# Optimization experiments

Measured on AMD Instinct MI355X. Metric: run time of the kernel, lower is better.

The kernel has to match this reference:

```python
import jax, jax.numpy as jnp
import numpy as np
import math

B, N, E, H, MLP_H = 4, 1024, 768, 12, 1536
D = E // H
EPS = 1e-6


def clayernorm(x, gamma, beta):
    # x: [..., E, 2]
    real, imag = x[..., 0], x[..., 1]
    mag = jnp.sqrt(real * real + imag * imag + EPS)
    mean = jnp.mean(mag, axis=-1, keepdims=True)
    var = jnp.mean((mag - mean) ** 2, axis=-1, keepdims=True)
    scale = ((mag - mean) / jnp.sqrt(var + EPS)) / (mag + EPS)
    out_r = gamma[:, 0] * (real * scale) + beta[:, 0]
    out_i = gamma[:, 1] * (imag * scale) + beta[:, 1]
    return jnp.stack([out_r, out_i], axis=-1)


def clinear(x, wr, wi, br, bi):
    # x: [..., in, 2]; wr/wi: [out, in]
    xr, xi = x[..., 0], x[..., 1]
    out_r = xr @ wr.T - xi @ wi.T + br
    out_i = xr @ wi.T + xi @ wr.T + bi
    return jnp.stack([out_r, out_i], axis=-1)


def cgelu(x):
    return jnp.stack([jax.nn.gelu(x[..., 0], approximate=False),
                      jax.nn.gelu(x[..., 1], approximate=False)], axis=-1)


def setup_inputs() -> dict:
    key = jax.random.key(0)
    ks = jax.random.split(key, 8)
    std_qkv = math.sqrt(2.0 / (E + 3 * E))
    std_proj = math.sqrt(2.0 / (E + E))
    std_m1 = math.sqrt(2.0 / (E + MLP_H))
    std_m2 = math.sqrt(2.0 / (MLP_H + E))
    return {
        "x": jax.random.normal(ks[0], (B, N, 2 * E), dtype=jnp.float32),
        "g1": jnp.ones((E, 2), jnp.float32), "b1": jnp.zeros((E, 2), jnp.float32),
        "g2": jnp.ones((E, 2), jnp.float32), "b2": jnp.zeros((E, 2), jnp.float32),
        "qkv_wr": std_qkv * jax.random.normal(ks[1], (3 * E, E), jnp.float32),
        "qkv_wi": std_qkv * jax.random.normal(ks[2], (3 * E, E), jnp.float32),
        "qkv_br": jnp.zeros((3 * E,), jnp.float32), "qkv_bi": jnp.zeros((3 * E,), jnp.float32),
        "proj_wr": std_proj * jax.random.normal(ks[3], (E, E), jnp.float32),
        "proj_wi": std_proj * jax.random.normal(ks[4], (E, E), jnp.float32),
        "proj_br": jnp.zeros((E,), jnp.float32), "proj_bi": jnp.zeros((E,), jnp.float32),
        "m1_wr": std_m1 * jax.random.normal(ks[5], (MLP_H, E), jnp.float32),
        "m1_wi": std_m1 * jax.random.normal(ks[6], (MLP_H, E), jnp.float32),
        "m1_br": jnp.zeros((MLP_H,), jnp.float32), "m1_bi": jnp.zeros((MLP_H,), jnp.float32),
        "m2_wr": std_m2 * jax.random.normal(ks[7], (E, MLP_H), jnp.float32),
        "m2_wi": std_m2 * jax.random.normal(jax.random.fold_in(key, 9), (E, MLP_H), jnp.float32),
        "m2_br": jnp.zeros((E,), jnp.float32), "m2_bi": jnp.zeros((E,), jnp.float32),
    }


def _forward(x, g1, b1, g2, b2, qkv_wr, qkv_wi, qkv_br, qkv_bi,
             proj_wr, proj_wi, proj_br, proj_bi,
             m1_wr, m1_wi, m1_br, m1_bi, m2_wr, m2_wi, m2_br, m2_bi):
    xc = x.reshape(B, N, E, 2)
    xn = clayernorm(xc, g1, b1)
    qkv = clinear(xn, qkv_wr, qkv_wi, qkv_br, qkv_bi)      # [B,N,3E,2]
    qkv = qkv.reshape(B, N, 3, H, D, 2).transpose(2, 0, 3, 1, 4, 5)  # [3,B,H,N,D,2]
    q, k, v = qkv[0], qkv[1], qkv[2]
    qr, qi = q[..., 0], q[..., 1]
    kr, ki = k[..., 0], k[..., 1]
    attn_r = jnp.einsum('bhqd,bhkd->bhqk', qr, kr) + jnp.einsum('bhqd,bhkd->bhqk', qi, ki)
    attn_i = jnp.einsum('bhqd,bhkd->bhqk', qr, ki) - jnp.einsum('bhqd,bhkd->bhqk', qi, kr)
    mag = jnp.sqrt(attn_r * attn_r + attn_i * attn_i + 1e-8) / math.sqrt(D)
    w = jax.nn.softmax(mag, axis=-1)
    out_r = jnp.einsum('bhqk,bhkd->bhqd', w, v[..., 0])
    out_i = jnp.einsum('bhqk,bhkd->bhqd', w, v[..., 1])
    attn_out = jnp.stack([out_r, out_i], axis=-1)           # [B,H,N,D,2]
    attn_out = attn_out.transpose(0, 2, 1, 3, 4).reshape(B, N, E, 2)
    attn_out = clinear(attn_out, proj_wr, proj_wi, proj_br, proj_bi)
    xc = xc + attn_out
    xn2 = clayernorm(xc, g2, b2)
    h = clinear(xn2, m1_wr, m1_wi, m1_br, m1_bi)
    h = cgelu(h)
    mlp_out = clinear(h, m2_wr, m2_wi, m2_br, m2_bi)
    xc = xc + mlp_out
    return xc.reshape(B, N, 2 * E)


def reference(x, g1, b1, g2, b2, qkv_wr, qkv_wi, qkv_br, qkv_bi,
              proj_wr, proj_wi, proj_br, proj_bi,
              m1_wr, m1_wi, m1_br, m1_bi, m2_wr, m2_wi, m2_br, m2_bi):
    return _forward(x, g1, b1, g2, b2, qkv_wr, qkv_wi, qkv_br, qkv_bi,
                    proj_wr, proj_wi, proj_br, proj_bi,
                    m1_wr, m1_wi, m1_br, m1_bi, m2_wr, m2_wi, m2_br, m2_bi)
```

## Files before the change

kernel.cpp:

```cpp
#include <hip/hip_runtime.h>
#include <math.h>

#define BB 4
#define NN 1024
#define EE 768
#define HH 12
#define DD 64
#define MLPH 1536
#define RR (BB*NN)
#define SZH ((size_t)48*1024*64)

constexpr float EPS = 1e-6f;

typedef __bf16 bf16_t;
typedef bf16_t bf16x8 __attribute__((ext_vector_type(8)));
typedef bf16_t bf16x4 __attribute__((ext_vector_type(4)));
typedef float  f32x4  __attribute__((ext_vector_type(4)));
typedef unsigned short us8 __attribute__((ext_vector_type(8)));

#define MFMA16 __builtin_amdgcn_mfma_f32_16x16x32_bf16

__device__ __forceinline__ float gelu_exact(float x){
  return 0.5f * x * (1.0f + erff(x * 0.70710678118654752440f));
}

__device__ __forceinline__ bf16x8 negv(bf16x8 v){
  us8 u = __builtin_bit_cast(us8, v);
  u ^= (unsigned short)0x8000;
  return __builtin_bit_cast(bf16x8, u);
}

__device__ __forceinline__ void split2(float f, bf16_t& h, bf16_t& l){
  h = (bf16_t)f; l = (bf16_t)(f - (float)h);
}

__device__ __forceinline__ void cvtstore(bf16_t* hp, bf16_t* lp, f32x4 v){
  bf16x4 h, l;
  #pragma unroll
  for (int i=0;i<4;i++){
    float f = v[i];
    bf16_t hb = (bf16_t)f;
    h[i] = hb;
    l[i] = (bf16_t)(f - (float)hb);
  }
  *(bf16x4*)hp = h;
  *(bf16x4*)lp = l;
}

__device__ __forceinline__ void gload_lds16(const bf16_t* g, bf16_t* l){
  __builtin_amdgcn_global_load_lds(
      (const __attribute__((address_space(1))) void*)g,
      (__attribute__((address_space(3))) void*)l, 16, 0, 0);
}

__device__ __forceinline__ size_t tiled_ad(int r, int c, int Ko){
  return (((size_t)(r>>4)*Ko + (c>>3))*16 + (r&15))*8 + (c&7);
}

__global__ __launch_bounds__(256) void cln_kernel(
    const float* __restrict__ inI,
    const float* __restrict__ inR, const float* __restrict__ inIm,
    const float* __restrict__ gamma, const float* __restrict__ beta,
    bf16_t* __restrict__ out4, int mode)
{
  const size_t PS = (size_t)RR*EE;
  int row = blockIdx.x;
  int t = threadIdx.x;
  __shared__ float sbuf[4];
  float vr[3], vi[3], mg[3];
  #pragma unroll
  for (int j=0;j<3;j++){
    int e = t + 256*j;
    float a, b;
    if (mode == 0){
      a = inI[(size_t)row*(2*EE) + 2*e];
      b = inI[(size_t)row*(2*EE) + 2*e + 1];
    } else {
      a = inR[(size_t)row*EE + e];
      b = inIm[(size_t)row*EE + e];
    }
    vr[j]=a; vi[j]=b;
    mg[j] = sqrtf(a*a + b*b + EPS);
  }
  int lane = t & 63, wv = t >> 6;
  float s = mg[0]+mg[1]+mg[2];
  #pragma unroll
  for (int o=32;o>0;o>>=1) s += __shfl_down(s, o, 64);
  if (lane==0) sbuf[wv] = s;
  __syncthreads();
  float mean = (sbuf[0]+sbuf[1]+sbuf[2]+sbuf[3]) * (1.0f/EE);
  __syncthreads();
  float v = 0.f;
  #pragma unroll
  for (int j=0;j<3;j++){ float d = mg[j]-mean; v += d*d; }
  #pragma unroll
  for (int o=32;o>0;o>>=1) v += __shfl_down(v, o, 64);
  if (lane==0) sbuf[wv] = v;
  __syncthreads();
  float var = (sbuf[0]+sbuf[1]+sbuf[2]+sbuf[3]) * (1.0f/EE);
  float inv = 1.0f / sqrtf(var + EPS);
  #pragma unroll
  for (int j=0;j<3;j++){
    int e = t + 256*j;
    float scale = ((mg[j]-mean) * inv) / (mg[j] + EPS);
    float oR = gamma[2*e]   * (vr[j]*scale) + beta[2*e];
    float oI = gamma[2*e+1] * (vi[j]*scale) + beta[2*e+1];
    bf16_t hR,lR,hI,lI;
    split2(oR,hR,lR); split2(oI,hI,lI);
    size_t ad = tiled_ad(row, e, 96);
    out4[ad]        = hR;
    out4[PS + ad]   = lR;
    out4[2*PS + ad] = hI;
    out4[3*PS + ad] = lI;
  }
}

template<int ACT, int RES_MODE, int OUT_MODE>
__global__ __launch_bounds__(256, 3) void cgemm_v3(
    const bf16_t* __restrict__ a4,
    const float* __restrict__ wr, const float* __restrict__ wi,
    const float* __restrict__ br_, const float* __restrict__ bi_,
    const float* __restrict__ resr, const float* __restrict__ resi,
    float* __restrict__ outr, float* __restrict__ outi,
    bf16_t* __restrict__ osplit,
    int K, int OUT)
{
  __shared__ bf16_t Al[16384];
  __shared__ bf16_t Bl[8192];

  const int tid = threadIdx.x;
  const int wid = tid >> 6, lane = tid & 63;
  const int rowBase = blockIdx.y * 128, colBase = blockIdx.x * 64;
  const int Ko = K >> 3;
  const size_t AS = (size_t)RR * K;

  const int b_so = (tid >> 4) & 3;
  const int b_se = (tid & 1) * 4;
  const int b_r0 = ((tid & 15) >> 1) + 8*wid;

  const int fr = lane & 15, fq = lane >> 4;
  const int wr0 = (wid >> 1) * 64, wc0 = (wid & 1) * 32;

  f32x4 accR[4][2], accI[4][2];
  #pragma unroll
  for (int mi=0;mi<4;mi++)
    #pragma unroll
    for (int ni=0;ni<2;ni++){ accR[mi][ni] = (f32x4)0.f; accI[mi][ni] = (f32x4)0.f; }

  f32x4 pBr[2], pBi[2];
  auto LOADB = [&](int k0){
    #pragma unroll
    for (int it=0; it<2; it++){
      size_t ro = (size_t)(colBase + b_r0 + it*32)*K + k0 + b_so*8 + b_se;
      pBr[it] = *(const f32x4*)(wr + ro);
      pBi[it] = *(const f32x4*)(wi + ro);
    }
  };
  LOADB(0);

  for (int k0 = 0; k0 < K; k0 += 32){
    const int o0 = k0 >> 3;
    __syncthreads();
    #pragma unroll
    for (int it=0; it<2; it++){
      int r = b_r0 + it*32;
      int off = ((r>>4)*4 + b_so)*128 + (r&15)*8 + b_se;
      cvtstore(&Bl[off],      &Bl[2048+off], pBr[it]);
      cvtstore(&Bl[4096+off], &Bl[6144+off], pBi[it]);
    }
    #pragma unroll
    for (int q=0; q<4; q++){
      #pragma unroll
      for (int s2=0; s2<2; s2++){
        int pi = wid*2 + s2;
        const bf16_t* g = a4 + (size_t)q*AS
            + ((size_t)(blockIdx.y*8 + pi)*Ko + o0)*128 + lane*8;
        gload_lds16(g, &Al[q*4096 + pi*512]);
      }
    }
    __syncthreads();
    if (k0 + 32 < K) LOADB(k0 + 32);

    bf16x8 brh[2], brl[2], bih[2], bil[2];
    #pragma unroll
    for (int ni=0; ni<2; ni++){
      int off = (((wid&1)*2 + ni)*4 + fq)*128 + fr*8;
      brh[ni] = *(const bf16x8*)&Bl[off];
      brl[ni] = *(const bf16x8*)&Bl[2048+off];
      bih[ni] = *(const bf16x8*)&Bl[4096+off];
      bil[ni] = *(const bf16x8*)&Bl[6144+off];
    }
    #pragma unroll
    for (int mi=0; mi<4; mi++){
      int off = (((wid>>1)*4 + mi)*4 + fq)*128 + fr*8;
      bf16x8 arh = *(const bf16x8*)&Al[off];
      bf16x8 arl = *(const bf16x8*)&Al[4096+off];
      bf16x8 aih = *(const bf16x8*)&Al[8192+off];
      bf16x8 ail = *(const bf16x8*)&Al[12288+off];
      bf16x8 nih = negv(aih), nil_ = negv(ail);
      #pragma unroll
      for (int ni=0; ni<2; ni++){
        f32x4 cR = accR[mi][ni], cI = accI[mi][ni];
        cR = MFMA16(arh,  brh[ni], cR, 0,0,0);
        cR = MFMA16(arh,  brl[ni], cR, 0,0,0);
        cR = MFMA16(arl,  brh[ni], cR, 0,0,0);
        cR = MFMA16(nih,  bih[ni], cR, 0,0,0);
        cR = MFMA16(nih,  bil[ni], cR, 0,0,0);
        cR = MFMA16(nil_, bih[ni], cR, 0,0,0);
        cI = MFMA16(arh,  bih[ni], cI, 0,0,0);
        cI = MFMA16(arh,  bil[ni], cI, 0,0,0);
        cI = MFMA16(arl,  bih[ni], cI, 0,0,0);
        cI = MFMA16(aih,  brh[ni], cI, 0,0,0);
        cI = MFMA16(aih,  brl[ni], cI, 0,0,0);
        cI = MFMA16(ail,  brh[ni], cI, 0,0,0);
        accR[mi][ni] = cR; accI[mi][ni] = cI;
      }
    }
  }

  const size_t OS = (size_t)RR * OUT;
  #pragma unroll
  for (int mi=0; mi<4; mi++){
    #pragma unroll
    for (int ni=0; ni<2; ni++){
      int c = colBase + wc0 + ni*16 + fr;
      float bR = br_[c], bI = bi_[c];
      #pragma unroll
      for (int j=0; j<4; j++){
        int r = rowBase + wr0 + mi*16 + fq*4 + j;
        float oR = accR[mi][ni][j] + bR;
        float oI = accI[mi][ni][j] + bI;
        if (ACT == 1){ oR = gelu_exact(oR); oI = gelu_exact(oI); }
        if (RES_MODE == 1){
          oR += resr[(size_t)r*OUT + c];
          oI += resi[(size_t)r*OUT + c];
        } else if (RES_MODE == 2){
          oR += resr[(size_t)r*(2*OUT) + 2*c];
          oI += resr[(size_t)r*(2*OUT) + 2*c + 1];
        }
        if (OUT_MODE == 0){
          outr[(size_t)r*OUT + c] = oR;
          outi[(size_t)r*OUT + c] = oI;
        } else if (OUT_MODE == 1){
          outr[(size_t)r*(2*OUT) + 2*c]     = oR;
          outr[(size_t)r*(2*OUT) + 2*c + 1] = oI;
        } else if (OUT_MODE == 2){
          int part = c / EE; int win = c - part*EE;
          int hh = win >> 6, dd = win & 63;
          int bq = r >> 10, nq = r & 1023;
          int bhh = bq*HH + hh;
          size_t idx = (part < 2) ? (((size_t)bhh*NN + nq)*DD + dd)
                                  : (((size_t)bhh*DD + dd)*NN + nq);
          bf16_t* bas = osplit + (size_t)part*4*SZH;
          bf16_t hR,lR,hI,lI;
          split2(oR,hR,lR); split2(oI,hI,lI);
          bas[idx]         = hR;
          bas[SZH + idx]   = lR;
          bas[2*SZH + idx] = hI;
          bas[3*SZH + idx] = lI;
        } else {
          bf16_t hR,lR,hI,lI;
          split2(oR,hR,lR); split2(oI,hI,lI);
          size_t ad = tiled_ad(r, c, OUT>>3);
          osplit[ad]        = hR;
          osplit[OS + ad]   = lR;
          osplit[2*OS + ad] = hI;
          osplit[3*OS + ad] = lI;
        }
      }
    }
  }
}

__global__ __launch_bounds__(256) void cattn_mfma(
    const bf16_t* __restrict__ qs,
    bf16_t* __restrict__ ao4)
{
  __shared__ bf16_t Krh[32][72], Krl[32][72], Kih[32][72], Kil[32][72];
  __shared__ bf16_t Vrh[64][40], Vrl[64][40], Vih[64][40], Vil[64][40];
  __shared__ bf16_t Pl[4][16][40];

  const int tid = threadIdx.x;
  const int lane = tid & 63, wid = tid >> 6;
  const int fr = lane & 15, fq = lane >> 4;
  const int qt = blockIdx.x, bh = blockIdx.y;
  const int b = bh / HH, h = bh - b*HH;

  const bf16_t* Qb = qs;
  const bf16_t* Kb = qs + 4*SZH;
  const bf16_t* Vb = qs + 8*SZH;

  const int qrow = qt*64 + wid*16 + fr;
  bf16x8 q_rh[2], q_rl[2], q_ih[2], q_il[2], nq_ih[2], nq_il[2];
  #pragma unroll
  for (int c=0;c<2;c++){
    size_t o = ((size_t)bh*NN + qrow)*DD + c*32 + fq*8;
    q_rh[c] = *(const bf16x8*)(Qb + 0*SZH + o);
    q_rl[c] = *(const bf16x8*)(Qb + 1*SZH + o);
    q_ih[c] = *(const bf16x8*)(Qb + 2*SZH + o);
    q_il[c] = *(const bf16x8*)(Qb + 3*SZH + o);
    nq_ih[c] = negv(q_ih[c]);
    nq_il[c] = negv(q_il[c]);
  }

  f32x4 accOr[4], accOi[4];
  #pragma unroll
  for (int df=0;df<4;df++){ accOr[df] = (f32x4)0.f; accOi[df] = (f32x4)0.f; }
  float m[4] = {0.f,0.f,0.f,0.f}, l[4] = {0.f,0.f,0.f,0.f};

  const int skr = tid >> 3, skc = (tid & 7) * 8;
  const int svr = tid >> 2, svc = (tid & 3) * 8;

  for (int kt = 0; kt < NN/32; kt++){
    __syncthreads();
    {
      size_t kb = ((size_t)bh*NN + kt*32 + skr)*DD + skc;
      *(bf16x8*)&Krh[skr][skc] = *(const bf16x8*)(Kb + 0*SZH + kb);
      *(bf16x8*)&Krl[skr][skc] = *(const bf16x8*)(Kb + 1*SZH + kb);
      *(bf16x8*)&Kih[skr][skc] = *(const bf16x8*)(Kb + 2*SZH + kb);
      *(bf16x8*)&Kil[skr][skc] = *(const bf16x8*)(Kb + 3*SZH + kb);
      size_t vb = ((size_t)bh*DD + svr)*NN + kt*32 + svc;
      *(bf16x8*)&Vrh[svr][svc] = *(const bf16x8*)(Vb + 0*SZH + vb);
      *(bf16x8*)&Vrl[svr][svc] = *(const bf16x8*)(Vb + 1*SZH + vb);
      *(bf16x8*)&Vih[svr][svc] = *(const bf16x8*)(Vb + 2*SZH + vb);
      *(bf16x8*)&Vil[svr][svc] = *(const bf16x8*)(Vb + 3*SZH + vb);
    }
    __syncthreads();

    f32x4 sr[2], si[2];
    #pragma unroll
    for (int f=0; f<2; f++){
      f32x4 r = (f32x4)0.f, im = (f32x4)0.f;
      #pragma unroll
      for (int c=0; c<2; c++){
        const int kr_ = f*16 + fr, co = c*32 + fq*8;
        bf16x8 krh = *(const bf16x8*)&Krh[kr_][co];
        bf16x8 krl = *(const bf16x8*)&Krl[kr_][co];
        bf16x8 kih = *(const bf16x8*)&Kih[kr_][co];
        bf16x8 kil = *(const bf16x8*)&Kil[kr_][co];
        r = MFMA16(q_rh[c], krh, r, 0,0,0);
        r = MFMA16(q_rh[c], krl, r, 0,0,0);
        r = MFMA16(q_rl[c], krh, r, 0,0,0);
        r = MFMA16(q_ih[c], kih, r, 0,0,0);
        r = MFMA16(q_ih[c], kil, r, 0,0,0);
        r = MFMA16(q_il[c], kih, r, 0,0,0);
        im = MFMA16(q_rh[c], kih, im, 0,0,0);
        im = MFMA16(q_rh[c], kil, im, 0,0,0);
        im = MFMA16(q_rl[c], kih, im, 0,0,0);
        im = MFMA16(nq_ih[c], krh, im, 0,0,0);
        im = MFMA16(nq_ih[c], krl, im, 0,0,0);
        im = MFMA16(nq_il[c], krh, im, 0,0,0);
      }
      sr[f] = r; si[f] = im;
    }

    float mg[2][4];
    #pragma unroll
    for (int f=0; f<2; f++)
      #pragma unroll
      for (int j=0; j<4; j++){
        float a = sr[f][j], c2 = si[f][j];
        mg[f][j] = sqrtf(fmaf(a,a, fmaf(c2,c2, 1e-8f))) * 0.125f;
      }
    float al[4];
    #pragma unroll
    for (int j=0; j<4; j++){
      float mx = fmaxf(mg[0][j], mg[1][j]);
      mx = fmaxf(mx, __shfl_xor(mx, 1, 64));
      mx = fmaxf(mx, __shfl_xor(mx, 2, 64));
      mx = fmaxf(mx, __shfl_xor(mx, 4, 64));
      mx = fmaxf(mx, __shfl_xor(mx, 8, 64));
      float nm = fmaxf(m[j], mx);
      al[j] = __expf(m[j] - nm);
      m[j] = nm;
    }
    unsigned pk[4]; float psum[4];
    #pragma unroll
    for (int j=0; j<4; j++){
      float p0 = __expf(mg[0][j] - m[j]);
      float p1 = __expf(mg[1][j] - m[j]);
      bf16_t b0 = (bf16_t)p0, b1 = (bf16_t)p1;
      pk[j] = (unsigned)__builtin_bit_cast(unsigned short, b0)
            | ((unsigned)__builtin_bit_cast(unsigned short, b1) << 16);
      psum[j] = (float)b0 + (float)b1;
    }
    #pragma unroll
    for (int j=0; j<4; j++){
      float s = psum[j];
      s += __shfl_xor(s, 1, 64);
      s += __shfl_xor(s, 2, 64);
      s += __shfl_xor(s, 4, 64);
      s += __shfl_xor(s, 8, 64);
      l[j] = l[j]*al[j] + s;
      #pragma unroll
      for (int df=0; df<4; df++){ accOr[df][j] *= al[j]; accOi[df][j] *= al[j]; }
    }
    #pragma unroll
    for (int j=0; j<4; j++){
      unsigned partner = (unsigned)__shfl_xor((int)pk[j], 1, 64);
      unsigned word; int kcol;
      if ((fr & 1) == 0){
        word = (pk[j] & 0xFFFFu) | (partner << 16);
        kcol = fr;
      } else {
        word = (partner >> 16) | (pk[j] & 0xFFFF0000u);
        kcol = 15 + fr;
      }
      int q = fq*4 + j;
      *(unsigned*)&Pl[wid][q][kcol] = word;
    }
    __syncthreads();

    bf16x8 pa = *(const bf16x8*)&Pl[wid][fr][fq*8];
    #pragma unroll
    for (int df=0; df<4; df++){
      const int dr = df*16 + fr, co = fq*8;
      bf16x8 vrh = *(const bf16x8*)&Vrh[dr][co];
      bf16x8 vrl = *(const bf16x8*)&Vrl[dr][co];
      bf16x8 vih = *(const bf16x8*)&Vih[dr][co];
      bf16x8 vil = *(const bf16x8*)&Vil[dr][co];
      f32x4 cr = accOr[df], ci = accOi[df];
      cr = MFMA16(pa, vrh, cr, 0,0,0);
      cr = MFMA16(pa, vrl, cr, 0,0,0);
      ci = MFMA16(pa, vih, ci, 0,0,0);
      ci = MFMA16(pa, vil, ci, 0,0,0);
      accOr[df] = cr; accOi[df] = ci;
    }
  }

  const size_t PS = (size_t)RR*EE;
  #pragma unroll
  for (int j=0; j<4; j++){
    float invl = 1.0f / l[j];
    int r = b*NN + qt*64 + wid*16 + fq*4 + j;
    #pragma unroll
    for (int df=0; df<4; df++){
      int c = h*DD + df*16 + fr;
      float vR = accOr[df][j] * invl;
      float vI = accOi[df][j] * invl;
      bf16_t hR,lR,hI,lI;
      split2(vR,hR,lR); split2(vI,hI,lI);
      size_t ad = tiled_ad(r, c, 96);
      ao4[ad]        = hR;
      ao4[PS + ad]   = lR;
      ao4[2*PS + ad] = hI;
      ao4[3*PS + ad] = lI;
    }
  }
}

extern "C" void kernel_launch(void* const* d_in, const int* in_sizes, int n_in,
                              void* d_out, int out_size, void* d_ws, size_t ws_size,
                              hipStream_t stream) {
  const float* x       = (const float*)d_in[0];
  const float* g1      = (const float*)d_in[1];
  const float* b1      = (const float*)d_in[2];
  const float* g2      = (const float*)d_in[3];
  const float* b2      = (const float*)d_in[4];
  const float* qkv_wr  = (const float*)d_in[5];
  const float* qkv_wi  = (const float*)d_in[6];
  const float* qkv_br  = (const float*)d_in[7];
  const float* qkv_bi  = (const float*)d_in[8];
  const float* proj_wr = (const float*)d_in[9];
  const float* proj_wi = (const float*)d_in[10];
  const float* proj_br = (const float*)d_in[11];
  const float* proj_bi = (const float*)d_in[12];
  const float* m1_wr   = (const float*)d_in[13];
  const float* m1_wi   = (const float*)d_in[14];
  const float* m1_br   = (const float*)d_in[15];
  const float* m1_bi   = (const float*)d_in[16];
  const float* m2_wr   = (const float*)d_in[17];
  const float* m2_wi   = (const float*)d_in[18];
  const float* m2_br   = (const float*)d_in[19];
  const float* m2_bi   = (const float*)d_in[20];

  float* ws = (float*)d_ws;
  const size_t RE = (size_t)RR * EE;
  bf16_t* xn4 = (bf16_t*)ws;
  bf16_t* ao4 = (bf16_t*)ws;
  bf16_t* qsplit = (bf16_t*)(ws + 2*RE);
  bf16_t* xn2_4  = (bf16_t*)(ws + 2*RE);
  bf16_t* h4     = (bf16_t*)(ws + 4*RE);
  float* x1_r  = ws + 8*RE;     float* x1_i  = ws + 9*RE;

  cln_kernel<<<RR, 256, 0, stream>>>(x, nullptr, nullptr, g1, b1, xn4, 0);
  cgemm_v3<0,0,2><<<dim3(36,32), 256, 0, stream>>>(
      xn4, qkv_wr, qkv_wi, qkv_br, qkv_bi,
      nullptr, nullptr, nullptr, nullptr, qsplit, EE, 3*EE);
  cattn_mfma<<<dim3(16,48), 256, 0, stream>>>(qsplit, ao4);
  cgemm_v3<0,2,0><<<dim3(12,32), 256, 0, stream>>>(
      ao4, proj_wr, proj_wi, proj_br, proj_bi,
      x, nullptr, x1_r, x1_i, nullptr, EE, EE);
  cln_kernel<<<RR, 256, 0, stream>>>(nullptr, x1_r, x1_i, g2, b2, xn2_4, 1);
  cgemm_v3<1,0,3><<<dim3(24,32), 256, 0, stream>>>(
      xn2_4, m1_wr, m1_wi, m1_br, m1_bi,
      nullptr, nullptr, nullptr, nullptr, h4, EE, MLPH);
  cgemm_v3<0,1,1><<<dim3(12,32), 256, 0, stream>>>(
      h4, m2_wr, m2_wi, m2_br, m2_bi,
      x1_r, x1_i, (float*)d_out, nullptr, nullptr, MLPH, EE);
}
```

Baseline: 884.1 us.

## Pre-tile K/V in fragment order and stage via direct global-to-LDS loads

The QKV GEMM epilogue now writes K and V split-bf16 planes in a per-32-key tiled layout that matches the MFMA fragment order. The attention kernel can then copy each tile with contiguous direct global-to-LDS 16-byte loads (gload_lds16) instead of going through registers into padded 2D shared arrays. The aim is to cut VGPR traffic and instruction count in the K/V staging loop and make the LDS fragment reads conflict-free. The unpadded layout could bring back LDS bank conflicts if the fragment ordering is off, and the scattered epilogue writes may cost more.

```diff
diff --git a/kernel.cpp b/kernel.cpp
--- a/kernel.cpp
+++ b/kernel.cpp
@@ -9,6 +9,7 @@
 #define MLPH 1536
 #define RR (BB*NN)
 #define SZH ((size_t)48*1024*64)
+#define BHSZ (NN*DD)
 
 constexpr float EPS = 1e-6f;
 
@@ -249,8 +250,16 @@
           int hh = win >> 6, dd = win & 63;
           int bq = r >> 10, nq = r & 1023;
           int bhh = bq*HH + hh;
-          size_t idx = (part < 2) ? (((size_t)bhh*NN + nq)*DD + dd)
-                                  : (((size_t)bhh*DD + dd)*NN + nq);
+          size_t idx;
+          if (part == 0){
+            idx = ((size_t)bhh*NN + nq)*DD + dd;
+          } else if (part == 1){
+            int kt = nq>>5, f = (nq>>4)&1, fro = nq&15, o = dd>>3, e = dd&7;
+            idx = (size_t)bhh*BHSZ + (size_t)kt*2048 + ((f*8+o)*16+fro)*8 + e;
+          } else {
+            int kt = nq>>5, df = dd>>4, fro = dd&15, o = (nq>>3)&3, e = nq&7;
+            idx = (size_t)bhh*BHSZ + (size_t)kt*2048 + ((df*4+o)*16+fro)*8 + e;
+          }
           bf16_t* bas = osplit + (size_t)part*4*SZH;
           bf16_t hR,lR,hI,lI;
           split2(oR,hR,lR); split2(oI,hI,lI);
@@ -276,8 +285,8 @@
     const bf16_t* __restrict__ qs,
     bf16_t* __restrict__ ao4)
 {
-  __shared__ bf16_t Krh[32][72], Krl[32][72], Kih[32][72], Kil[32][72];
-  __shared__ bf16_t Vrh[64][40], Vrl[64][40], Vih[64][40], Vil[64][40];
+  __shared__ bf16_t Kl[8192];
+  __shared__ bf16_t Vl[8192];
   __shared__ bf16_t Pl[4][16][40];
 
   const int tid = threadIdx.x;
@@ -308,22 +317,15 @@
   for (int df=0;df<4;df++){ accOr[df] = (f32x4)0.f; accOi[df] = (f32x4)0.f; }
   float m[4] = {0.f,0.f,0.f,0.f}, l[4] = {0.f,0.f,0.f,0.f};
 
-  const int skr = tid >> 3, skc = (tid & 7) * 8;
-  const int svr = tid >> 2, svc = (tid & 3) * 8;
-
   for (int kt = 0; kt < NN/32; kt++){
     __syncthreads();
     {
-      size_t kb = ((size_t)bh*NN + kt*32 + skr)*DD + skc;
-      *(bf16x8*)&Krh[skr][skc] = *(const bf16x8*)(Kb + 0*SZH + kb);
-      *(bf16x8*)&Krl[skr][skc] = *(const bf16x8*)(Kb + 1*SZH + kb);
-      *(bf16x8*)&Kih[skr][skc] = *(const bf16x8*)(Kb + 2*SZH + kb);
-      *(bf16x8*)&Kil[skr][skc] = *(const bf16x8*)(Kb + 3*SZH + kb);
-      size_t vb = ((size_t)bh*DD + svr)*NN + kt*32 + svc;
-      *(bf16x8*)&Vrh[svr][svc] = *(const bf16x8*)(Vb + 0*SZH + vb);
-      *(bf16x8*)&Vrl[svr][svc] = *(const bf16x8*)(Vb + 1*SZH + vb);
-      *(bf16x8*)&Vih[svr][svc] = *(const bf16x8*)(Vb + 2*SZH + vb);
-      *(bf16x8*)&Vil[svr][svc] = *(const bf16x8*)(Vb + 3*SZH + vb);
+      const size_t base = (size_t)bh*BHSZ + (size_t)kt*2048 + wid*512 + lane*8;
+      #pragma unroll
+      for (int q=0; q<4; q++){
+        gload_lds16(Kb + q*SZH + base, &Kl[q*2048 + wid*512]);
+        gload_lds16(Vb + q*SZH + base, &Vl[q*2048 + wid*512]);
+      }
     }
     __syncthreads();
 
@@ -333,11 +335,11 @@
       f32x4 r = (f32x4)0.f, im = (f32x4)0.f;
       #pragma unroll
       for (int c=0; c<2; c++){
-        const int kr_ = f*16 + fr, co = c*32 + fq*8;
-        bf16x8 krh = *(const bf16x8*)&Krh[kr_][co];
-        bf16x8 krl = *(const bf16x8*)&Krl[kr_][co];
-        bf16x8 kih = *(const bf16x8*)&Kih[kr_][co];
-        bf16x8 kil = *(const bf16x8*)&Kil[kr_][co];
+        const int off = ((f*8 + c*4 + fq)*16 + fr)*8;
+        bf16x8 krh = *(const bf16x8*)&Kl[off];
+        bf16x8 krl = *(const bf16x8*)&Kl[2048+off];
+        bf16x8 kih = *(const bf16x8*)&Kl[4096+off];
+        bf16x8 kil = *(const bf16x8*)&Kl[6144+off];
         r = MFMA16(q_rh[c], krh, r, 0,0,0);
         r = MFMA16(q_rh[c], krl, r, 0,0,0);
         r = MFMA16(q_rl[c], krh, r, 0,0,0);
@@ -414,11 +416,11 @@
     bf16x8 pa = *(const bf16x8*)&Pl[wid][fr][fq*8];
     #pragma unroll
     for (int df=0; df<4; df++){
-      const int dr = df*16 + fr, co = fq*8;
-      bf16x8 vrh = *(const bf16x8*)&Vrh[dr][co];
-      bf16x8 vrl = *(const bf16x8*)&Vrl[dr][co];
-      bf16x8 vih = *(const bf16x8*)&Vih[dr][co];
-      bf16x8 vil = *(const bf16x8*)&Vil[dr][co];
+      const int off = ((df*4 + fq)*16 + fr)*8;
+      bf16x8 vrh = *(const bf16x8*)&Vl[off];
+      bf16x8 vrl = *(const bf16x8*)&Vl[2048+off];
+      bf16x8 vih = *(const bf16x8*)&Vl[4096+off];
+      bf16x8 vil = *(const bf16x8*)&Vl[6144+off];
       f32x4 cr = accOr[df], ci = accOi[df];
       cr = MFMA16(pa, vrh, cr, 0,0,0);
       cr = MFMA16(pa, vrl, cr, 0,0,0);
```

Measured after the change: 896.4 us. Within noise of the previous version (+1.4%).
